# Optimization experiments

Measured on AMD Instinct MI355X. Metric: run time of the kernel, lower is better.

The kernel has to match this reference:

```python
import jax, jax.numpy as jnp
import numpy as np

B, T, I, H, O = 2048, 72, 200, 200, 53
EPS = 1e-5


def _gru_layer(x, h0, Wih, Whh, bih, bhh):
    """PyTorch-convention GRU. x: [B,T,I], h0: [B,H]. Gate order: r, z, n."""
    xW = jnp.einsum('bti,gi->btg', x, Wih) + bih  # [B,T,3H] precomputed input proj

    def step(h, xw):
        hw = h @ Whh.T + bhh                       # [B,3H]
        xr, xz, xn = jnp.split(xw, 3, axis=-1)
        hr, hz, hn = jnp.split(hw, 3, axis=-1)
        r = jax.nn.sigmoid(xr + hr)
        z = jax.nn.sigmoid(xz + hz)
        n = jnp.tanh(xn + r * hn)
        h_new = (1.0 - z) * n + z * h
        return h_new, h_new

    hT, ys = jax.lax.scan(step, h0, jnp.swapaxes(xW, 0, 1))  # ys: [T,B,H]
    return jnp.swapaxes(ys, 0, 1), hT


def setup_inputs() -> dict:
    key = jax.random.key(0)
    ks = jax.random.split(key, 16)
    s = 0.05
    inp = {
        'encoded': jax.random.normal(ks[0], (B, I), dtype=jnp.float32),
        'hidden_1': jnp.zeros((1, B, H), dtype=jnp.float32),
        'hidden_2': jnp.zeros((1, B, H), dtype=jnp.float32),
        'hidden_3': jnp.zeros((1, B, H), dtype=jnp.float32),
        # BatchNorm1d (eval mode: running stats)
        'bn_gamma': jnp.ones((I,), jnp.float32),
        'bn_beta': jnp.zeros((I,), jnp.float32),
        'bn_mean': jnp.zeros((I,), jnp.float32),
        'bn_var': jnp.ones((I,), jnp.float32),
        'fc_in_W': jax.random.normal(ks[1], (H, I), jnp.float32) * s,
        'fc_in_b': jnp.zeros((H,), jnp.float32),
        'Wih1': jax.random.normal(ks[2], (3 * H, I), jnp.float32) * s,
        'Whh1': jax.random.normal(ks[3], (3 * H, H), jnp.float32) * s,
        'bih1': jnp.zeros((3 * H,), jnp.float32),
        'bhh1': jnp.zeros((3 * H,), jnp.float32),
        'Wih2': jax.random.normal(ks[4], (3 * H, H), jnp.float32) * s,
        'Whh2': jax.random.normal(ks[5], (3 * H, H), jnp.float32) * s,
        'bih2': jnp.zeros((3 * H,), jnp.float32),
        'bhh2': jnp.zeros((3 * H,), jnp.float32),
        'Wih3': jax.random.normal(ks[6], (3 * H, H), jnp.float32) * s,
        'Whh3': jax.random.normal(ks[7], (3 * H, H), jnp.float32) * s,
        'bih3': jnp.zeros((3 * H,), jnp.float32),
        'bhh3': jnp.zeros((3 * H,), jnp.float32),
        'fc_out_W': jax.random.normal(ks[8], (O, H), jnp.float32) * s,
        'fc_out_b': jnp.zeros((O,), jnp.float32),
    }
    return inp


def reference(encoded, hidden_1, hidden_2, hidden_3, bn_gamma, bn_beta, bn_mean,
              bn_var, fc_in_W, fc_in_b, Wih1, Whh1, bih1, bhh1, Wih2, Whh2,
              bih2, bhh2, Wih3, Whh3, bih3, bhh3, fc_out_W, fc_out_b):
    # BatchNorm1d (eval) -> Linear -> ReLU
    xh = (encoded - bn_mean) * jax.lax.rsqrt(bn_var + EPS) * bn_gamma + bn_beta
    emb = jax.nn.relu(xh @ fc_in_W.T + fc_in_b)              # [B,H]
    embedded = jnp.broadcast_to(emb[:, None, :], (B, T, H))  # repeat over T

    out1, h1 = _gru_layer(embedded, hidden_1[0], Wih1, Whh1, bih1, bhh1)
    out2, h2 = _gru_layer(out1, hidden_2[0], Wih2, Whh2, bih2, bhh2)
    out3, h3 = _gru_layer(out2, hidden_3[0], Wih3, Whh3, bih3, bhh3)

    out = jnp.einsum('bth,oh->bto', out3, fc_out_W) + fc_out_b  # [B,T,O]
    out = jax.nn.relu(jax.nn.sigmoid(out))
    return out, h1[None], h2[None], h3[None]
```

## Files before the change

### kernel.cpp

```cpp
#include <hip/hip_runtime.h>

typedef _Float16 half8 __attribute__((ext_vector_type(8)));
typedef float f32x4 __attribute__((ext_vector_type(4)));

namespace {
constexpr int kB = 2048;
constexpr int kT = 72;
constexpr int kI = 200;
constexpr int kH = 200;
constexpr int kO = 53;
constexpr int kG = 600;
constexpr int BT = 8;
constexpr int NWG = kB / BT;
constexpr int MT = 38;
constexpr int KS = 7;
constexpr int GSTR = 18;

constexpr int XW1    = 0;
constexpr int WIH1T  = 1228800;
constexpr int FCINT  = 1348800;
constexpr int F0     = 1388800;
constexpr int FSZ    = 68096;
constexpr int FHEAD  = F0 + 5 * FSZ;
constexpr int PERM   = MT * KS * 64;

constexpr int OH1 = kB * kT * kO;
constexpr int OH2 = OH1 + kB * kH;
constexpr int OH3 = OH2 + kB * kH;
}

__device__ __forceinline__ float sig_(float x) { return 1.0f / (1.0f + __expf(-x)); }
__device__ __forceinline__ float tanh_(float x) {
    return 1.0f - 2.0f / (__expf(2.0f * x) + 1.0f);
}

__device__ __forceinline__ void barx() {
    asm volatile("s_waitcnt lgkmcnt(0)\n\ts_barrier" ::: "memory");
}

__device__ __forceinline__ void store_fb(_Float16* fb, int n, int j, float v) {
    int ks = j >> 5, r = j & 31;
    fb[((ks << 6) + ((r >> 3) << 4) + n) * 8 + (r & 7)] = (_Float16)v;
}


__global__ __launch_bounds__(256) void prep_transpose2(
    const float* __restrict__ Wih1, const float* __restrict__ fciW,
    float* __restrict__ ws) {
    int idx = blockIdx.x * 256 + threadIdx.x;
    if (idx < 120000) {
        int k = idx / kG, c = idx - k * kG;
        ws[WIH1T + idx] = Wih1[c * kI + k];
    } else {
        int i = idx - 120000;
        if (i < 40000) {
            int k = i / kH, h = i - k * kH;
            ws[FCINT + i] = fciW[h * kI + k];
        }
    }
}

__global__ __launch_bounds__(256) void prep_frags(
    const float* __restrict__ Whh1, const float* __restrict__ Wih2,
    const float* __restrict__ Whh2, const float* __restrict__ Wih3,
    const float* __restrict__ Whh3, const float* __restrict__ fcoW,
    float* __restrict__ ws) {
    int idx = blockIdx.x * 256 + threadIdx.x;
    const float* src; int R; long long dstHalf; int rem;
    if (idx < 5 * PERM) {
        int m = idx / PERM; rem = idx - m * PERM;
        switch (m) {
            case 0: src = Whh1; break;
            case 1: src = Wih2; break;
            case 2: src = Whh2; break;
            case 3: src = Wih3; break;
            default: src = Whh3; break;
        }
        R = kG; dstHalf = 2LL * (F0 + m * FSZ);
    } else {
        rem = idx - 5 * PERM;
        if (rem >= 4 * KS * 64) return;
        src = fcoW; R = kO; dstHalf = 2LL * FHEAD;
    }
    int lane = rem & 63;
    int tmp = rem >> 6;
    int ks = tmp % KS;
    int mt = tmp / KS;
    int row = mt * 16 + (lane & 15);
    int k0 = ks * 32 + (lane >> 4) * 8;
    half8 v;
    #pragma unroll
    for (int j = 0; j < 8; ++j) {
        int k = k0 + j;
        v[j] = (_Float16)((row < R && k < kH) ? src[row * kH + k] : 0.0f);
    }
    *(half8*)((_Float16*)ws + dstHalf + (long long)rem * 8) = v;
}

__global__ __launch_bounds__(256) void prep_input(
    const float* __restrict__ enc,
    const float* __restrict__ bn_g, const float* __restrict__ bn_b,
    const float* __restrict__ bn_m, const float* __restrict__ bn_v,
    const float* __restrict__ fcib, const float* __restrict__ bih1,
    float* ws) {
    __shared__ float xh[kI];
    __shared__ float emb[kH];
    const int b = blockIdx.x, tid = threadIdx.x;
    const float* fcInT = ws + FCINT;
    const float* Wih1T = ws + WIH1T;
    if (tid < kI) {
        float x = enc[b * kI + tid];
        xh[tid] = (x - bn_m[tid]) * rsqrtf(bn_v[tid] + 1e-5f) * bn_g[tid] + bn_b[tid];
    }
    __syncthreads();
    if (tid < kH) {
        float s = fcib[tid];
        for (int k = 0; k < kI; ++k) s = fmaf(xh[k], fcInT[k * kH + tid], s);
        emb[tid] = fmaxf(s, 0.0f);
    }
    __syncthreads();
    for (int c = tid; c < kG; c += 256) {
        float s = bih1[c];
        for (int k = 0; k < kH; ++k) s = fmaf(emb[k], Wih1T[k * kG + c], s);
        ws[XW1 + b * kG + c] = s;
    }
}

__global__ __launch_bounds__(1024, 4) void gru_main(
    const float* __restrict__ ws,
    const float* __restrict__ h1in, const float* __restrict__ h2in,
    const float* __restrict__ h3in,
    const float* __restrict__ bhh1,
    const float* __restrict__ bih2, const float* __restrict__ bhh2,
    const float* __restrict__ bih3, const float* __restrict__ bhh3,
    const float* __restrict__ fcob,
    float* __restrict__ out) {
    __shared__ float xwL[kG * BT];
    __shared__ __align__(16) _Float16 fb1[KS * 64 * 8];
    __shared__ __align__(16) _Float16 fb2[KS * 64 * 8];
    __shared__ __align__(16) _Float16 fb3[KS * 64 * 8];
    __shared__ __align__(16) _Float16 whdL[4 * KS * 64 * 8];
    __shared__ float Gs[608 * GSTR];
    __shared__ float Gns[208 * GSTR];
    __shared__ float bias[9 * kH];
    __shared__ float hb[64];

    const int tid = threadIdx.x, wv = tid >> 6, ln = tid & 63;
    const int lb = ln >> 4, lr = ln & 15;
    const int b0 = blockIdx.x * BT;
    const bool lo = (ln < 16);
    half8 z8;
    #pragma unroll
    for (int j = 0; j < 8; ++j) z8[j] = (_Float16)0.0f;

    {
        float4* f1 = (float4*)fb1;
        float4* f2 = (float4*)fb2;
        float4* f3 = (float4*)fb3;
        const float4 z4 = {0.f, 0.f, 0.f, 0.f};
        for (int i = tid; i < KS * 64 * 8 * 2 / 16; i += 1024) {
            f1[i] = z4; f2[i] = z4; f3[i] = z4;
        }
    }
    {
        const half8* src = (const half8*)(ws + FHEAD);
        for (int i = tid; i < 4 * KS * 64; i += 1024)
            *(half8*)(whdL + (long long)i * 8) = src[i];
    }
    for (int i = tid; i < kG * BT; i += 1024) {
        int n = i / kG, j = i - n * kG;
        float v = ws[XW1 + (b0 + n) * kG + j];
        if (j < 2 * kH) v += bhh1[j];
        xwL[j * BT + n] = v;
    }
    for (int i = tid; i < 9 * kH; i += 1024) {
        int c = i / kH, j = i - c * kH;
        float v;
        switch (c) {
            case 0:  v = bhh1[2 * kH + j]; break;
            case 1:  v = bih2[j] + bhh2[j]; break;
            case 2:  v = bih2[kH + j] + bhh2[kH + j]; break;
            case 3:  v = bih2[2 * kH + j]; break;
            case 4:  v = bhh2[2 * kH + j]; break;
            case 5:  v = bih3[j] + bhh3[j]; break;
            case 6:  v = bih3[kH + j] + bhh3[kH + j]; break;
            case 7:  v = bih3[2 * kH + j]; break;
            default: v = bhh3[2 * kH + j]; break;
        }
        bias[i] = v;
    }
    if (tid < 64) hb[tid] = (tid < kO) ? fcob[tid] : 0.0f;
    __syncthreads();

    float h1r[2], h2r[2], h3r[2];
    #pragma unroll
    for (int s = 0; s < 2; ++s) {
        int idx = tid + s * 1024;
        if (idx < BT * kH) {
            int n = idx & 7, j = idx >> 3;
            h1r[s] = h1in[(b0 + n) * kH + j];
            h2r[s] = h2in[(b0 + n) * kH + j];
            h3r[s] = h3in[(b0 + n) * kH + j];
            store_fb(fb1, n, j, h1r[s]);
            store_fb(fb2, n, j, h2r[s]);
            store_fb(fb3, n, j, h3r[s]);
        } else { h1r[s] = h2r[s] = h3r[s] = 0.0f; }
    }
    __syncthreads();

    const half8* WFhh1 = (const half8*)(ws + F0);
    const half8* WFih2 = (const half8*)(ws + F0 + FSZ);
    const half8* WFhh2 = (const half8*)(ws + F0 + 2 * FSZ);
    const half8* WFih3 = (const half8*)(ws + F0 + 3 * FSZ);
    const half8* WFhh3 = (const half8*)(ws + F0 + 4 * FSZ);

    for (int t = 0; t < kT; ++t) {
        if (wv >= 4) {
            half8 bf[KS];
            #pragma unroll
            for (int ks = 0; ks < KS; ++ks)
                bf[ks] = *(const half8*)(fb1 + (ks * 64 + ln) * 8);
            for (int mt = wv - 4; mt < MT; mt += 12) {
                const half8* wp = WFhh1 + (mt * KS) * 64 + ln;
                f32x4 acc = {0.f, 0.f, 0.f, 0.f};
                #pragma unroll
                for (int ks = 0; ks < KS - 1; ++ks)
                    acc = __builtin_amdgcn_mfma_f32_16x16x32_f16(wp[ks * 64], bf[ks], acc, 0, 0, 0);
                half8 w6 = z8;
                if (lo) w6 = wp[(KS - 1) * 64];
                acc = __builtin_amdgcn_mfma_f32_16x16x32_f16(w6, bf[KS - 1], acc, 0, 0, 0);
                int row = mt * 16 + lb * 4;
                #pragma unroll
                for (int rg = 0; rg < 4; ++rg) Gs[(row + rg) * GSTR + lr] = acc[rg];
            }
        } else if (t > 0) {
            f32x4 acc = {0.f, 0.f, 0.f, 0.f};
            #pragma unroll
            for (int ks = 0; ks < KS; ++ks) {
                half8 w = *(const half8*)(whdL + ((wv * KS + ks) * 64 + ln) * 8);
                half8 b = *(const half8*)(fb3 + (ks * 64 + ln) * 8);
                acc = __builtin_amdgcn_mfma_f32_16x16x32_f16(w, b, acc, 0, 0, 0);
            }
            if (lr < BT) {
                int o0 = wv * 16 + lb * 4;
                int obase = (b0 + lr) * (kT * kO) + (t - 1) * kO;
                #pragma unroll
                for (int rg = 0; rg < 4; ++rg) {
                    int o = o0 + rg;
                    if (o < kO) out[obase + o] = sig_(acc[rg] + hb[o]);
                }
            }
        }
        barx();
        #pragma unroll
        for (int s = 0; s < 2; ++s) {
            int idx = tid + s * 1024;
            if (idx < BT * kH) {
                int n = idx & 7, j = idx >> 3;
                float r  = sig_(xwL[j * BT + n]            + Gs[j * GSTR + n]);
                float z  = sig_(xwL[(kH + j) * BT + n]     + Gs[(kH + j) * GSTR + n]);
                float nn = tanh_(xwL[(2 * kH + j) * BT + n] + r * (Gs[(2 * kH + j) * GSTR + n] + bias[j]));
                h1r[s] = (1.0f - z) * nn + z * h1r[s];
                store_fb(fb1, n, j, h1r[s]);
            }
        }
        barx();
        {
            half8 bx[KS], bh[KS];
            #pragma unroll
            for (int ks = 0; ks < KS; ++ks) {
                bx[ks] = *(const half8*)(fb1 + (ks * 64 + ln) * 8);
                bh[ks] = *(const half8*)(fb2 + (ks * 64 + ln) * 8);
            }
            for (int mt = wv; mt < MT; mt += 16) {
                const half8* wpx = WFih2 + (mt * KS) * 64 + ln;
                const half8* wph = WFhh2 + (mt * KS) * 64 + ln;
                f32x4 ax = {0.f, 0.f, 0.f, 0.f}, ah = {0.f, 0.f, 0.f, 0.f};
                #pragma unroll
                for (int ks = 0; ks < KS - 1; ++ks) {
                    ax = __builtin_amdgcn_mfma_f32_16x16x32_f16(wpx[ks * 64], bx[ks], ax, 0, 0, 0);
                    ah = __builtin_amdgcn_mfma_f32_16x16x32_f16(wph[ks * 64], bh[ks], ah, 0, 0, 0);
                }
                half8 wx6 = z8, wh6 = z8;
                if (lo) { wx6 = wpx[(KS - 1) * 64]; wh6 = wph[(KS - 1) * 64]; }
                ax = __builtin_amdgcn_mfma_f32_16x16x32_f16(wx6, bx[KS - 1], ax, 0, 0, 0);
                ah = __builtin_amdgcn_mfma_f32_16x16x32_f16(wh6, bh[KS - 1], ah, 0, 0, 0);
                int row = mt * 16 + lb * 4;
                if (mt < 25) {
                    #pragma unroll
                    for (int rg = 0; rg < 4; ++rg) Gs[(row + rg) * GSTR + lr] = ax[rg] + ah[rg];
                } else {
                    #pragma unroll
                    for (int rg = 0; rg < 4; ++rg) {
                        Gs[(row + rg) * GSTR + lr] = ax[rg];
                        Gns[(row - 400 + rg) * GSTR + lr] = ah[rg];
                    }
                }
            }
        }
        barx();
        #pragma unroll
        for (int s = 0; s < 2; ++s) {
            int idx = tid + s * 1024;
            if (idx < BT * kH) {
                int n = idx & 7, j = idx >> 3;
                float r  = sig_(Gs[j * GSTR + n]            + bias[kH + j]);
                float z  = sig_(Gs[(kH + j) * GSTR + n]     + bias[2 * kH + j]);
                float nn = tanh_(Gs[(2 * kH + j) * GSTR + n] + bias[3 * kH + j]
                                 + r * (Gns[j * GSTR + n]   + bias[4 * kH + j]));
                h2r[s] = (1.0f - z) * nn + z * h2r[s];
                store_fb(fb2, n, j, h2r[s]);
            }
        }
        barx();
        {
            half8 bx[KS], bh[KS];
            #pragma unroll
            for (int ks = 0; ks < KS; ++ks) {
                bx[ks] = *(const half8*)(fb2 + (ks * 64 + ln) * 8);
                bh[ks] = *(const half8*)(fb3 + (ks * 64 + ln) * 8);
            }
            for (int mt = wv; mt < MT; mt += 16) {
                const half8* wpx = WFih3 + (mt * KS) * 64 + ln;
                const half8* wph = WFhh3 + (mt * KS) * 64 + ln;
                f32x4 ax = {0.f, 0.f, 0.f, 0.f}, ah = {0.f, 0.f, 0.f, 0.f};
                #pragma unroll
                for (int ks = 0; ks < KS - 1; ++ks) {
                    ax = __builtin_amdgcn_mfma_f32_16x16x32_f16(wpx[ks * 64], bx[ks], ax, 0, 0, 0);
                    ah = __builtin_amdgcn_mfma_f32_16x16x32_f16(wph[ks * 64], bh[ks], ah, 0, 0, 0);
                }
                half8 wx6 = z8, wh6 = z8;
                if (lo) { wx6 = wpx[(KS - 1) * 64]; wh6 = wph[(KS - 1) * 64]; }
                ax = __builtin_amdgcn_mfma_f32_16x16x32_f16(wx6, bx[KS - 1], ax, 0, 0, 0);
                ah = __builtin_amdgcn_mfma_f32_16x16x32_f16(wh6, bh[KS - 1], ah, 0, 0, 0);
                int row = mt * 16 + lb * 4;
                if (mt < 25) {
                    #pragma unroll
                    for (int rg = 0; rg < 4; ++rg) Gs[(row + rg) * GSTR + lr] = ax[rg] + ah[rg];
                } else {
                    #pragma unroll
                    for (int rg = 0; rg < 4; ++rg) {
                        Gs[(row + rg) * GSTR + lr] = ax[rg];
                        Gns[(row - 400 + rg) * GSTR + lr] = ah[rg];
                    }
                }
            }
        }
        barx();
        #pragma unroll
        for (int s = 0; s < 2; ++s) {
            int idx = tid + s * 1024;
            if (idx < BT * kH) {
                int n = idx & 7, j = idx >> 3;
                float r  = sig_(Gs[j * GSTR + n]            + bias[5 * kH + j]);
                float z  = sig_(Gs[(kH + j) * GSTR + n]     + bias[6 * kH + j]);
                float nn = tanh_(Gs[(2 * kH + j) * GSTR + n] + bias[7 * kH + j]
                                 + r * (Gns[j * GSTR + n]   + bias[8 * kH + j]));
                h3r[s] = (1.0f - z) * nn + z * h3r[s];
                store_fb(fb3, n, j, h3r[s]);
            }
        }
        barx();
    }

    if (wv < 4) {
        f32x4 acc = {0.f, 0.f, 0.f, 0.f};
        #pragma unroll
        for (int ks = 0; ks < KS; ++ks) {
            half8 w = *(const half8*)(whdL + ((wv * KS + ks) * 64 + ln) * 8);
            half8 b = *(const half8*)(fb3 + (ks * 64 + ln) * 8);
            acc = __builtin_amdgcn_mfma_f32_16x16x32_f16(w, b, acc, 0, 0, 0);
        }
        if (lr < BT) {
            int o0 = wv * 16 + lb * 4;
            int obase = (b0 + lr) * (kT * kO) + (kT - 1) * kO;
            #pragma unroll
            for (int rg = 0; rg < 4; ++rg) {
                int o = o0 + rg;
                if (o < kO) out[obase + o] = sig_(acc[rg] + hb[o]);
            }
        }
    }

    #pragma unroll
    for (int s = 0; s < 2; ++s) {
        int idx = tid + s * 1024;
        if (idx < BT * kH) {
            Gs[idx] = h1r[s];
            Gs[1600 + idx] = h2r[s];
            Gs[3200 + idx] = h3r[s];
        }
    }
    __syncthreads();
    for (int i = tid; i < BT * kH; i += 1024) {
        int n = i / kH, j = i - n * kH;
        int src = j * BT + n;
        out[OH1 + (b0 + n) * kH + j] = Gs[src];
        out[OH2 + (b0 + n) * kH + j] = Gs[1600 + src];
        out[OH3 + (b0 + n) * kH + j] = Gs[3200 + src];
    }
}

extern "C" void kernel_launch(void* const* d_in, const int* in_sizes, int n_in,
                              void* d_out, int out_size, void* d_ws, size_t ws_size,
                              hipStream_t stream) {
    (void)in_sizes; (void)n_in; (void)out_size; (void)ws_size;
    const float* enc  = (const float*)d_in[0];
    const float* h1in = (const float*)d_in[1];
    const float* h2in = (const float*)d_in[2];
    const float* h3in = (const float*)d_in[3];
    const float* bn_g = (const float*)d_in[4];
    const float* bn_b = (const float*)d_in[5];
    const float* bn_m = (const float*)d_in[6];
    const float* bn_v = (const float*)d_in[7];
    const float* fciW = (const float*)d_in[8];
    const float* fcib = (const float*)d_in[9];
    const float* Wih1 = (const float*)d_in[10];
    const float* Whh1 = (const float*)d_in[11];
    const float* bih1 = (const float*)d_in[12];
    const float* bhh1 = (const float*)d_in[13];
    const float* Wih2 = (const float*)d_in[14];
    const float* Whh2 = (const float*)d_in[15];
    const float* bih2 = (const float*)d_in[16];
    const float* bhh2 = (const float*)d_in[17];
    const float* Wih3 = (const float*)d_in[18];
    const float* Whh3 = (const float*)d_in[19];
    const float* bih3 = (const float*)d_in[20];
    const float* bhh3 = (const float*)d_in[21];
    const float* fcoW = (const float*)d_in[22];
    const float* fcob = (const float*)d_in[23];
    float* ws  = (float*)d_ws;
    float* out = (float*)d_out;

    hipLaunchKernelGGL(prep_transpose2, dim3(625), dim3(256), 0, stream, Wih1, fciW, ws);
    hipLaunchKernelGGL(prep_frags, dim3(340), dim3(256), 0, stream,
                       Whh1, Wih2, Whh2, Wih3, Whh3, fcoW, ws);
    hipLaunchKernelGGL(prep_input, dim3(kB), dim3(256), 0, stream,
                       enc, bn_g, bn_b, bn_m, bn_v, fcib, bih1, ws);
    hipLaunchKernelGGL(gru_main, dim3(NWG), dim3(1024), 0, stream,
                       ws, h1in, h2in, h3in, bhh1, bih2, bhh2, bih3, bhh3, fcob, out);
}
```

Measured before the change: 1.103 ms.

## Software-pipeline layer-1 recurrence into layer-2 phase to cut per-step barriers

Layer 1's hidden-state matmul and gate update for step t+1 are computed in the same phase as layer 2's step t, reusing the fb1 operand already loaded. The output head also moves into that phase, and its weights are now read from global memory instead of an LDS copy. This removes two barriers and one serial phase per timestep. In exchange, the layer-2 phase carries more work, a separate Gs1 buffer is needed (more LDS, which may lower occupancy), and the head weights are no longer served from LDS.

New measurement: 1.108 ms. Within noise of the previous version (+0.5%).

```diff
diff --git a/kernel.cpp b/kernel.cpp
--- a/kernel.cpp
+++ b/kernel.cpp
@@ -139,8 +139,8 @@
     __shared__ __align__(16) _Float16 fb1[KS * 64 * 8];
     __shared__ __align__(16) _Float16 fb2[KS * 64 * 8];
     __shared__ __align__(16) _Float16 fb3[KS * 64 * 8];
-    __shared__ __align__(16) _Float16 whdL[4 * KS * 64 * 8];
     __shared__ float Gs[608 * GSTR];
+    __shared__ float Gs1[608 * GSTR];
     __shared__ float Gns[208 * GSTR];
     __shared__ float bias[9 * kH];
     __shared__ float hb[64];
@@ -161,11 +161,6 @@
         for (int i = tid; i < KS * 64 * 8 * 2 / 16; i += 1024) {
             f1[i] = z4; f2[i] = z4; f3[i] = z4;
         }
-    }
-    {
-        const half8* src = (const half8*)(ws + FHEAD);
-        for (int i = tid; i < 4 * KS * 64; i += 1024)
-            *(half8*)(whdL + (long long)i * 8) = src[i];
     }
     for (int i = tid; i < kG * BT; i += 1024) {
         int n = i / kG, j = i - n * kG;
@@ -213,58 +208,44 @@
     const half8* WFhh2 = (const half8*)(ws + F0 + 2 * FSZ);
     const half8* WFih3 = (const half8*)(ws + F0 + 3 * FSZ);
     const half8* WFhh3 = (const half8*)(ws + F0 + 4 * FSZ);
+    const half8* WFhead = (const half8*)(ws + FHEAD);
+
+    {
+        half8 bf[KS];
+        #pragma unroll
+        for (int ks = 0; ks < KS; ++ks)
+            bf[ks] = *(const half8*)(fb1 + (ks * 64 + ln) * 8);
+        for (int mt = wv; mt < MT; mt += 16) {
+            const half8* wp = WFhh1 + (mt * KS) * 64 + ln;
+            f32x4 acc = {0.f, 0.f, 0.f, 0.f};
+            #pragma unroll
+            for (int ks = 0; ks < KS - 1; ++ks)
+                acc = __builtin_amdgcn_mfma_f32_16x16x32_f16(wp[ks * 64], bf[ks], acc, 0, 0, 0);
+            half8 w6 = z8;
+            if (lo) w6 = wp[(KS - 1) * 64];
+            acc = __builtin_amdgcn_mfma_f32_16x16x32_f16(w6, bf[KS - 1], acc, 0, 0, 0);
+            int row = mt * 16 + lb * 4;
+            #pragma unroll
+            for (int rg = 0; rg < 4; ++rg) Gs1[(row + rg) * GSTR + lr] = acc[rg];
+        }
+    }
+    barx();
+    #pragma unroll
+    for (int s = 0; s < 2; ++s) {
+        int idx = tid + s * 1024;
+        if (idx < BT * kH) {
+            int n = idx & 7, j = idx >> 3;
+            float r  = sig_(xwL[j * BT + n]            + Gs1[j * GSTR + n]);
+            float z  = sig_(xwL[(kH + j) * BT + n]     + Gs1[(kH + j) * GSTR + n]);
+            float nn = tanh_(xwL[(2 * kH + j) * BT + n] + r * (Gs1[(2 * kH + j) * GSTR + n] + bias[j]));
+            h1r[s] = (1.0f - z) * nn + z * h1r[s];
+            store_fb(fb1, n, j, h1r[s]);
+        }
+    }
+    barx();
 
     for (int t = 0; t < kT; ++t) {
-        if (wv >= 4) {
-            half8 bf[KS];
-            #pragma unroll
-            for (int ks = 0; ks < KS; ++ks)
-                bf[ks] = *(const half8*)(fb1 + (ks * 64 + ln) * 8);
-            for (int mt = wv - 4; mt < MT; mt += 12) {
-                const half8* wp = WFhh1 + (mt * KS) * 64 + ln;
-                f32x4 acc = {0.f, 0.f, 0.f, 0.f};
-                #pragma unroll
-                for (int ks = 0; ks < KS - 1; ++ks)
-                    acc = __builtin_amdgcn_mfma_f32_16x16x32_f16(wp[ks * 64], bf[ks], acc, 0, 0, 0);
-                half8 w6 = z8;
-                if (lo) w6 = wp[(KS - 1) * 64];
-                acc = __builtin_amdgcn_mfma_f32_16x16x32_f16(w6, bf[KS - 1], acc, 0, 0, 0);
-                int row = mt * 16 + lb * 4;
-                #pragma unroll
-                for (int rg = 0; rg < 4; ++rg) Gs[(row + rg) * GSTR + lr] = acc[rg];
-            }
-        } else if (t > 0) {
-            f32x4 acc = {0.f, 0.f, 0.f, 0.f};
-            #pragma unroll
-            for (int ks = 0; ks < KS; ++ks) {
-                half8 w = *(const half8*)(whdL + ((wv * KS + ks) * 64 + ln) * 8);
-                half8 b = *(const half8*)(fb3 + (ks * 64 + ln) * 8);
-                acc = __builtin_amdgcn_mfma_f32_16x16x32_f16(w, b, acc, 0, 0, 0);
-            }
-            if (lr < BT) {
-                int o0 = wv * 16 + lb * 4;
-                int obase = (b0 + lr) * (kT * kO) + (t - 1) * kO;
-                #pragma unroll
-                for (int rg = 0; rg < 4; ++rg) {
-                    int o = o0 + rg;
-                    if (o < kO) out[obase + o] = sig_(acc[rg] + hb[o]);
-                }
-            }
-        }
-        barx();
-        #pragma unroll
-        for (int s = 0; s < 2; ++s) {
-            int idx = tid + s * 1024;
-            if (idx < BT * kH) {
-                int n = idx & 7, j = idx >> 3;
-                float r  = sig_(xwL[j * BT + n]            + Gs[j * GSTR + n]);
-                float z  = sig_(xwL[(kH + j) * BT + n]     + Gs[(kH + j) * GSTR + n]);
-                float nn = tanh_(xwL[(2 * kH + j) * BT + n] + r * (Gs[(2 * kH + j) * GSTR + n] + bias[j]));
-                h1r[s] = (1.0f - z) * nn + z * h1r[s];
-                store_fb(fb1, n, j, h1r[s]);
-            }
-        }
-        barx();
+        const bool doM1 = (t + 1 < kT);
         {
             half8 bx[KS], bh[KS];
             #pragma unroll
@@ -272,28 +253,72 @@
                 bx[ks] = *(const half8*)(fb1 + (ks * 64 + ln) * 8);
                 bh[ks] = *(const half8*)(fb2 + (ks * 64 + ln) * 8);
             }
-            for (int mt = wv; mt < MT; mt += 16) {
-                const half8* wpx = WFih2 + (mt * KS) * 64 + ln;
-                const half8* wph = WFhh2 + (mt * KS) * 64 + ln;
-                f32x4 ax = {0.f, 0.f, 0.f, 0.f}, ah = {0.f, 0.f, 0.f, 0.f};
-                #pragma unroll
-                for (int ks = 0; ks < KS - 1; ++ks) {
-                    ax = __builtin_amdgcn_mfma_f32_16x16x32_f16(wpx[ks * 64], bx[ks], ax, 0, 0, 0);
-                    ah = __builtin_amdgcn_mfma_f32_16x16x32_f16(wph[ks * 64], bh[ks], ah, 0, 0, 0);
-                }
-                half8 wx6 = z8, wh6 = z8;
-                if (lo) { wx6 = wpx[(KS - 1) * 64]; wh6 = wph[(KS - 1) * 64]; }
-                ax = __builtin_amdgcn_mfma_f32_16x16x32_f16(wx6, bx[KS - 1], ax, 0, 0, 0);
-                ah = __builtin_amdgcn_mfma_f32_16x16x32_f16(wh6, bh[KS - 1], ah, 0, 0, 0);
-                int row = mt * 16 + lb * 4;
-                if (mt < 25) {
+            for (int item = wv; item < 80; item += 16) {
+                if (item < 38) {
+                    const int mt = item;
+                    const half8* wpx = WFih2 + (mt * KS) * 64 + ln;
+                    const half8* wph = WFhh2 + (mt * KS) * 64 + ln;
+                    f32x4 ax = {0.f, 0.f, 0.f, 0.f}, ah = {0.f, 0.f, 0.f, 0.f};
                     #pragma unroll
-                    for (int rg = 0; rg < 4; ++rg) Gs[(row + rg) * GSTR + lr] = ax[rg] + ah[rg];
+                    for (int ks = 0; ks < KS - 1; ++ks) {
+                        ax = __builtin_amdgcn_mfma_f32_16x16x32_f16(wpx[ks * 64], bx[ks], ax, 0, 0, 0);
+                        ah = __builtin_amdgcn_mfma_f32_16x16x32_f16(wph[ks * 64], bh[ks], ah, 0, 0, 0);
+                    }
+                    half8 wx6 = z8, wh6 = z8;
+                    if (lo) { wx6 = wpx[(KS - 1) * 64]; wh6 = wph[(KS - 1) * 64]; }
+                    ax = __builtin_amdgcn_mfma_f32_16x16x32_f16(wx6, bx[KS - 1], ax, 0, 0, 0);
+                    ah = __builtin_amdgcn_mfma_f32_16x16x32_f16(wh6, bh[KS - 1], ah, 0, 0, 0);
+                    int row = mt * 16 + lb * 4;
+                    if (mt < 25) {
+                        #pragma unroll
+                        for (int rg = 0; rg < 4; ++rg) Gs[(row + rg) * GSTR + lr] = ax[rg] + ah[rg];
+                    } else {
+                        #pragma unroll
+                        for (int rg = 0; rg < 4; ++rg) {
+                            Gs[(row + rg) * GSTR + lr] = ax[rg];
+                            Gns[(row - 400 + rg) * GSTR + lr] = ah[rg];
+                        }
+                    }
+                } else if (item < 76) {
+                    if (doM1) {
+                        const int mt = item - 38;
+                        const half8* wp = WFhh1 + (mt * KS) * 64 + ln;
+                        f32x4 acc = {0.f, 0.f, 0.f, 0.f};
+                        #pragma unroll
+                        for (int ks = 0; ks < KS - 1; ++ks)
+                            acc = __builtin_amdgcn_mfma_f32_16x16x32_f16(wp[ks * 64], bx[ks], acc, 0, 0, 0);
+                        half8 w6 = z8;
+                        if (lo) w6 = wp[(KS - 1) * 64];
+                        acc = __builtin_amdgcn_mfma_f32_16x16x32_f16(w6, bx[KS - 1], acc, 0, 0, 0);
+                        int row = mt * 16 + lb * 4;
+                        #pragma unroll
+                        for (int rg = 0; rg < 4; ++rg) Gs1[(row + rg) * GSTR + lr] = acc[rg];
+                    }
                 } else {
-                    #pragma unroll
-                    for (int rg = 0; rg < 4; ++rg) {
-                        Gs[(row + rg) * GSTR + lr] = ax[rg];
-                        Gns[(row - 400 + rg) * GSTR + lr] = ah[rg];
+                    if (t > 0) {
+                        const int hw = item - 76;
+                        const half8* wp = WFhead + (hw * KS) * 64 + ln;
+                        f32x4 acc = {0.f, 0.f, 0.f, 0.f};
+                        #pragma unroll
+                        for (int ks = 0; ks < KS - 1; ++ks) {
+                            half8 b = *(const half8*)(fb3 + (ks * 64 + ln) * 8);
+                            acc = __builtin_amdgcn_mfma_f32_16x16x32_f16(wp[ks * 64], b, acc, 0, 0, 0);
+                        }
+                        {
+                            half8 w6 = z8;
+                            if (lo) w6 = wp[(KS - 1) * 64];
+                            half8 b = *(const half8*)(fb3 + ((KS - 1) * 64 + ln) * 8);
+                            acc = __builtin_amdgcn_mfma_f32_16x16x32_f16(w6, b, acc, 0, 0, 0);
+                        }
+                        if (lr < BT) {
+                            int o0 = hw * 16 + lb * 4;
+                            int obase = (b0 + lr) * (kT * kO) + (t - 1) * kO;
+                            #pragma unroll
+                            for (int rg = 0; rg < 4; ++rg) {
+                                int o = o0 + rg;
+                                if (o < kO) out[obase + o] = sig_(acc[rg] + hb[o]);
+                            }
+                        }
                     }
                 }
             }
@@ -310,6 +335,20 @@
                                  + r * (Gns[j * GSTR + n]   + bias[4 * kH + j]));
                 h2r[s] = (1.0f - z) * nn + z * h2r[s];
                 store_fb(fb2, n, j, h2r[s]);
+            }
+        }
+        if (doM1) {
+            #pragma unroll
+            for (int s = 0; s < 2; ++s) {
+                int idx = tid + s * 1024;
+                if (idx < BT * kH) {
+                    int n = idx & 7, j = idx >> 3;
+                    float r  = sig_(xwL[j * BT + n]            + Gs1[j * GSTR + n]);
+                    float z  = sig_(xwL[(kH + j) * BT + n]     + Gs1[(kH + j) * GSTR + n]);
+                    float nn = tanh_(xwL[(2 * kH + j) * BT + n] + r * (Gs1[(2 * kH + j) * GSTR + n] + bias[j]));
+                    h1r[s] = (1.0f - z) * nn + z * h1r[s];
+                    store_fb(fb1, n, j, h1r[s]);
+                }
             }
         }
         barx();
@@ -364,12 +403,18 @@
     }
 
     if (wv < 4) {
+        const half8* wp = WFhead + (wv * KS) * 64 + ln;
         f32x4 acc = {0.f, 0.f, 0.f, 0.f};
         #pragma unroll
-        for (int ks = 0; ks < KS; ++ks) {
-            half8 w = *(const half8*)(whdL + ((wv * KS + ks) * 64 + ln) * 8);
+        for (int ks = 0; ks < KS - 1; ++ks) {
             half8 b = *(const half8*)(fb3 + (ks * 64 + ln) * 8);
-            acc = __builtin_amdgcn_mfma_f32_16x16x32_f16(w, b, acc, 0, 0, 0);
+            acc = __builtin_amdgcn_mfma_f32_16x16x32_f16(wp[ks * 64], b, acc, 0, 0, 0);
+        }
+        {
+            half8 w6 = z8;
+            if (lo) w6 = wp[(KS - 1) * 64];
+            half8 b = *(const half8*)(fb3 + ((KS - 1) * 64 + ln) * 8);
+            acc = __builtin_amdgcn_mfma_f32_16x16x32_f16(w6, b, acc, 0, 0, 0);
         }
         if (lr < BT) {
             int o0 = wv * 16 + lb * 4;
```
